# Kernel optimization log

Measured on AMD Instinct MI355X. Metric: run time of the kernel, lower is better.

The kernel has to match this reference:

```python
import jax, jax.numpy as jnp
import numpy as np

B, N, IN_DIM, HID, HEADS, K = 2, 2048, 1024, 512, 8, 8
HD = HID // HEADS
EPS = 1e-5
SCALE = float(1.0 / np.sqrt(HD))

def _ln(x, g, b):
    m = jnp.mean(x, -1, keepdims=True)
    v = jnp.var(x, -1, keepdims=True)
    return (x - m) * jax.lax.rsqrt(v + EPS) * g + b

def setup_inputs() -> dict:
    key = jax.random.key(0)
    ks = jax.random.split(key, 40)
    def p(k, shape):
        return jax.random.normal(k, shape, jnp.float32) * 0.02
    z = lambda *s: jnp.zeros(s, jnp.float32)
    o = lambda *s: jnp.ones(s, jnp.float32)
    return {
        "x": jax.random.normal(ks[0], (B, N, IN_DIM), jnp.float32),
        # fc_start: Linear(in,hid) + GLU Linear(hid,2*hid)
        "w_start": p(ks[1], (HID, IN_DIM)), "b_start": z(HID),
        "glu_w": p(ks[2], (2 * HID, HID)), "glu_b": z(2 * HID),
        # 2 GCN layers (stacked on leading axis)
        "gcn_w": p(ks[3], (2, HID, HID)), "gcn_b": z(2, HID),
        "gcn_g": o(2, HID), "gcn_beta": z(2, HID),
        # 2 transformer layers
        "qkv_w": p(ks[4], (2, 3 * HID, HID)), "qkv_b": z(2, 3 * HID),
        "out_w": p(ks[5], (2, HID, HID)), "out_b": z(2, HID),
        "ln1_g": o(2, HID), "ln1_b": z(2, HID),
        "ffn_w1": p(ks[6], (2, 2 * HID, HID)), "ffn_b1": z(2, 2 * HID),
        "ffn_w2": p(ks[7], (2, HID, 2 * HID)), "ffn_b2": z(2, HID),
        "ln2_g": o(2, HID), "ln2_b": z(2, HID),
        # fusion, attention pooling, classifier
        "fus_w": p(ks[8], (HID, 2 * HID)), "fus_b": z(HID),
        "attn_w1": p(ks[9], (256, HID)), "attn_b1": z(256),
        "attn_w2": p(ks[10], (1, 256)), "attn_b2": z(1),
        "cls_w1": p(ks[11], (HID // 2, HID)), "cls_b1": z(HID // 2),
        "cls_w2": p(ks[12], (1, HID // 2)), "cls_b2": z(1),
    }

def reference(x, w_start, b_start, glu_w, glu_b, gcn_w, gcn_b, gcn_g, gcn_beta,
              qkv_w, qkv_b, out_w, out_b, ln1_g, ln1_b, ffn_w1, ffn_b1,
              ffn_w2, ffn_b2, ln2_g, ln2_b, fus_w, fus_b,
              attn_w1, attn_b1, attn_w2, attn_b2,
              cls_w1, cls_b1, cls_w2, cls_b2):
    # fc_start: Linear -> GLU (dropout off in eval)
    h = x @ w_start.T + b_start
    vg = h @ glu_w.T + glu_b
    val, gate = jnp.split(vg, 2, -1)
    h = val * jax.nn.sigmoid(gate)                      # [B,N,HID]

    # dynamic KNN graph: cdist + topk + scatter + sym-normalize
    sq = jnp.sum(h * h, -1)
    d2 = sq[:, :, None] + sq[:, None, :] - 2.0 * jnp.einsum('bnc,bmc->bnm', h, h)
    dist = jnp.sqrt(jnp.maximum(d2, 0.0))
    _, idx = jax.lax.top_k(-dist, K + 1)                # nearest K+1 (incl self)
    bi = jnp.arange(B)[:, None, None]
    ri = jnp.arange(N)[None, :, None]
    adj = jnp.zeros((B, N, N), h.dtype).at[bi, ri, idx].set(1.0)
    rs = jnp.sum(adj, -1)
    dinv = jnp.where(rs > 0, rs ** -0.5, 0.0)
    adj = adj * dinv[:, :, None] * dinv[:, None, :]     # == D^-1/2 A D^-1/2

    # GCN branch
    hg = h
    for i in range(2):
        s = hg @ gcn_w[i].T + gcn_b[i]
        o = jnp.einsum('bnm,bmc->bnc', adj, s)
        o = _ln(o, gcn_g[i], gcn_beta[i])
        hg = jax.nn.leaky_relu(o, 0.2) + hg

    # Transformer branch (post-LN)
    ht = h
    for i in range(2):
        qkv = ht @ qkv_w[i].T + qkv_b[i]
        q, k_, v = jnp.split(qkv, 3, -1)
        q = q.reshape(B, N, HEADS, HD)
        k_ = k_.reshape(B, N, HEADS, HD)
        v = v.reshape(B, N, HEADS, HD)
        att = jax.nn.softmax(jnp.einsum('bqhd,bkhd->bhqk', q, k_) * SCALE, -1)
        ao = jnp.einsum('bhqk,bkhd->bqhd', att, v).reshape(B, N, HID)
        ao = ao @ out_w[i].T + out_b[i]
        ht = _ln(ht + ao, ln1_g[i], ln1_b[i])
        ff = jax.nn.gelu(ht @ ffn_w1[i].T + ffn_b1[i], approximate=False) @ ffn_w2[i].T + ffn_b2[i]
        ht = _ln(ht + ff, ln2_g[i], ln2_b[i])

    hf = jnp.concatenate([hg, ht], -1) @ fus_w.T + fus_b  # [B,N,HID]

    # gated attention pooling
    a = jnp.tanh(hf @ attn_w1.T + attn_b1) @ attn_w2.T + attn_b2
    a = jax.nn.softmax(a, axis=1)                       # [B,N,1]
    M = jnp.sum(hf * a, axis=1)                         # [B,HID]

    logits = jax.nn.elu(M @ cls_w1.T + cls_b1) @ cls_w2.T + cls_b2  # [B,1]
    return logits, a, M
```

## Files before the change

### kernel.cpp

```cpp
#include <hip/hip_runtime.h>
#include <hip/hip_bf16.h>
#include <math.h>

#define NSEQ 2048
#define ROWS 4096
#define KNN 9
#define MB (1ull << 20)

typedef short bh8 __attribute__((ext_vector_type(8)));
typedef float f4v __attribute__((ext_vector_type(4)));
typedef unsigned long long u64k;

__device__ __forceinline__ short f2bf(float f) {
    union { float f; unsigned u; } v; v.f = f;
    unsigned r = (v.u + 0x7fffu + ((v.u >> 16) & 1u)) >> 16;
    return (short)r;
}
__device__ __forceinline__ float b2f(short s) {
    union { unsigned u; float f; } v; v.u = ((unsigned)(unsigned short)s) << 16; return v.f;
}

__device__ __forceinline__ void gload16(const void* g, void* l) {
    __builtin_amdgcn_global_load_lds(
        (const __attribute__((address_space(1))) void*)g,
        (__attribute__((address_space(3))) void*)l, 16, 0, 0);
}

__device__ __forceinline__ float blockReduceSum(float v, float* red) {
    int tid = threadIdx.x;
    red[tid] = v; __syncthreads();
    for (int s = 128; s > 0; s >>= 1) {
        if (tid < s) red[tid] += red[tid + s];
        __syncthreads();
    }
    float r = red[0]; __syncthreads();
    return r;
}

struct CvtArgs { const float* src[10]; short* dst[10]; int n4[10]; };
__global__ __launch_bounds__(256) void cvt_k(CvtArgs a) {
    int s = blockIdx.y;
    const float* sp = a.src[s]; short* dp = a.dst[s]; int n = a.n4[s];
    for (int i = blockIdx.x * 256 + threadIdx.x; i < n; i += gridDim.x * 256) {
        float4 v = ((const float4*)sp)[i];
        short4 o; o.x = f2bf(v.x); o.y = f2bf(v.y); o.z = f2bf(v.z); o.w = f2bf(v.w);
        ((short4*)dp)[i] = o;
    }
}

template <int OUTMODE>
__global__ __launch_bounds__(256) void mfma_gemm(
        const short* __restrict__ A, const short* __restrict__ W,
        const float* __restrict__ bias, float* __restrict__ Cf, short* __restrict__ Cb,
        int M, int N, int K)
{
    __shared__ short As[2][64 * 64];
    __shared__ short Bs[2][64 * 64];
    int tid = threadIdx.x;
    int wv = tid >> 6, l = tid & 63;
    int g = l >> 4, c = l & 15;
    int wr = wv >> 1, wc = wv & 1;
    int bm = blockIdx.y * 64, bn = blockIdx.x * 64;
    int sr = l >> 3, sc = ((l & 7) ^ sr) * 8;
    const short* Ap = A + (size_t)(bm + wv * 16 + sr) * K + sc;
    const short* Wp = W + (size_t)(bn + wv * 16 + sr) * K + sc;
    int ldsB = (wv * 16) * 64;

    #define GSTAGE(buf, k0) { \
        gload16(Ap + (k0), &As[buf][ldsB]); \
        gload16(Ap + (size_t)8 * K + (k0), &As[buf][ldsB + 8 * 64]); \
        gload16(Wp + (k0), &Bs[buf][ldsB]); \
        gload16(Wp + (size_t)8 * K + (k0), &Bs[buf][ldsB + 8 * 64]); }

    f4v acc[2][2] = {};
    GSTAGE(0, 0);
    __syncthreads();
    int nk = K >> 6;
    for (int t = 0; t < nk; ++t) {
        int cur = t & 1;
        if (t + 1 < nk) GSTAGE(cur ^ 1, (t + 1) << 6);
        #pragma unroll
        for (int ks = 0; ks < 2; ++ks) {
            bh8 af[2], bf_[2];
            #pragma unroll
            for (int mi = 0; mi < 2; ++mi) {
                int row = wr * 32 + mi * 16 + c;
                af[mi] = *(const bh8*)(&As[cur][row * 64 + (((ks * 4 + g) ^ (c & 7)) * 8)]);
            }
            #pragma unroll
            for (int ni = 0; ni < 2; ++ni) {
                int row = wc * 32 + ni * 16 + c;
                bf_[ni] = *(const bh8*)(&Bs[cur][row * 64 + (((ks * 4 + g) ^ (c & 7)) * 8)]);
            }
            #pragma unroll
            for (int mi = 0; mi < 2; ++mi)
                #pragma unroll
                for (int ni = 0; ni < 2; ++ni)
                    acc[mi][ni] = __builtin_amdgcn_mfma_f32_16x16x32_bf16(af[mi], bf_[ni], acc[mi][ni], 0, 0, 0);
        }
        __syncthreads();
    }
    #undef GSTAGE
    short* Kb_  = (OUTMODE == 3) ? Cb + 2097152 : nullptr;
    short* Vt_  = (OUTMODE == 3) ? Cb + 4194304 : nullptr;
    #pragma unroll
    for (int mi = 0; mi < 2; ++mi) {
        int row = bm + wr * 32 + mi * 16 + g * 4;
        #pragma unroll
        for (int ni = 0; ni < 2; ++ni) {
            int col = bn + wc * 32 + ni * 16 + c;
            float bv = bias[col];
            if (OUTMODE == 3) {
                int b = row >> 11, n0 = row & 2047;
                if (col < 512) {
                    int h = col >> 6, d = col & 63;
                    size_t base = (((size_t)(b * 8 + h) * NSEQ + n0) << 6) + d;
                    #pragma unroll
                    for (int rr = 0; rr < 4; ++rr)
                        Cb[base + ((size_t)rr << 6)] = f2bf((acc[mi][ni][rr] + bv) * 0.18033688f);
                } else if (col < 1024) {
                    int cc = col - 512, h = cc >> 6, d = cc & 63;
                    size_t base = (((size_t)(b * 8 + h) * NSEQ + n0) << 6) + d;
                    #pragma unroll
                    for (int rr = 0; rr < 4; ++rr)
                        Kb_[base + ((size_t)rr << 6)] = f2bf(acc[mi][ni][rr] + bv);
                } else {
                    int cc = col - 1024, h = cc >> 6, d = cc & 63;
                    short4 ov;
                    ov.x = f2bf(acc[mi][ni][0] + bv);
                    ov.y = f2bf(acc[mi][ni][1] + bv);
                    ov.z = f2bf(acc[mi][ni][2] + bv);
                    ov.w = f2bf(acc[mi][ni][3] + bv);
                    *(short4*)(Vt_ + (((size_t)((b * 8 + h) * 64 + d)) << 11) + n0) = ov;
                }
            } else {
                #pragma unroll
                for (int rr = 0; rr < 4; ++rr) {
                    float v = acc[mi][ni][rr] + bv;
                    if (OUTMODE == 0) Cf[(size_t)(row + rr) * N + col] = v;
                    else if (OUTMODE == 1) Cb[(size_t)(row + rr) * N + col] = f2bf(v);
                    else if (OUTMODE == 2) {
                        Cf[(size_t)(row + rr) * N + col] = v;
                        Cb[(size_t)(row + rr) * N + col] = f2bf(v);
                    } else if (OUTMODE == 4) {
                        Cb[(size_t)(row + rr) * N + col] = f2bf(0.5f * v * (1.f + erff(v * 0.70710678118654752f)));
                    } else if (OUTMODE == 5) {
                        Cf[(size_t)(row + rr) * N + col] = tanhf(v);
                    }
                }
            }
        }
    }
}

__global__ __launch_bounds__(256) void mfma_gram(
        const short* __restrict__ Hi, const short* __restrict__ Lo,
        const float* __restrict__ SQ, float* __restrict__ D2)
{
    __shared__ short HiR[64 * 64], LoR[64 * 64], HiC[64 * 64], LoC[64 * 64];
    int tid = threadIdx.x;
    int wv = tid >> 6, l = tid & 63;
    int g = l >> 4, c = l & 15;
    int wr = wv >> 1, wc = wv & 1;
    int bm = blockIdx.y * 64, bn = blockIdx.x * 64;
    int sr = l >> 3, sc = ((l & 7) ^ sr) * 8;
    const short* hiR = Hi + (size_t)(bm + wv * 16 + sr) * 512 + sc;
    const short* loR = Lo + (size_t)(bm + wv * 16 + sr) * 512 + sc;
    const short* hiC = Hi + (size_t)(bn + wv * 16 + sr) * 512 + sc;
    const short* loC = Lo + (size_t)(bn + wv * 16 + sr) * 512 + sc;
    int ldsOff = (wv * 16) * 64;
    f4v acc[2][2] = {};
    for (int k0 = 0; k0 < 512; k0 += 64) {
        __syncthreads();
        gload16(hiR + k0, HiR + ldsOff);
        gload16(hiR + (size_t)8 * 512 + k0, HiR + ldsOff + 8 * 64);
        gload16(loR + k0, LoR + ldsOff);
        gload16(loR + (size_t)8 * 512 + k0, LoR + ldsOff + 8 * 64);
        gload16(hiC + k0, HiC + ldsOff);
        gload16(hiC + (size_t)8 * 512 + k0, HiC + ldsOff + 8 * 64);
        gload16(loC + k0, LoC + ldsOff);
        gload16(loC + (size_t)8 * 512 + k0, LoC + ldsOff + 8 * 64);
        __syncthreads();
        #pragma unroll
        for (int ks = 0; ks < 2; ++ks) {
            bh8 hr[2], lr_[2], hc[2], lc[2];
            #pragma unroll
            for (int mi = 0; mi < 2; ++mi) {
                int o = (wr * 32 + mi * 16 + c) * 64 + (((ks * 4 + g) ^ (c & 7)) * 8);
                hr[mi] = *(const bh8*)(HiR + o);
                lr_[mi] = *(const bh8*)(LoR + o);
            }
            #pragma unroll
            for (int ni = 0; ni < 2; ++ni) {
                int o = (wc * 32 + ni * 16 + c) * 64 + (((ks * 4 + g) ^ (c & 7)) * 8);
                hc[ni] = *(const bh8*)(HiC + o);
                lc[ni] = *(const bh8*)(LoC + o);
            }
            #pragma unroll
            for (int mi = 0; mi < 2; ++mi)
                #pragma unroll
                for (int ni = 0; ni < 2; ++ni) {
                    acc[mi][ni] = __builtin_amdgcn_mfma_f32_16x16x32_bf16(hr[mi], hc[ni], acc[mi][ni], 0, 0, 0);
                    acc[mi][ni] = __builtin_amdgcn_mfma_f32_16x16x32_bf16(hr[mi], lc[ni], acc[mi][ni], 0, 0, 0);
                    acc[mi][ni] = __builtin_amdgcn_mfma_f32_16x16x32_bf16(lr_[mi], hc[ni], acc[mi][ni], 0, 0, 0);
                }
        }
    }
    #pragma unroll
    for (int mi = 0; mi < 2; ++mi) {
        int row = bm + wr * 32 + mi * 16 + g * 4;
        #pragma unroll
        for (int ni = 0; ni < 2; ++ni) {
            int col = bn + wc * 32 + ni * 16 + c;
            float sqc = SQ[col];
            #pragma unroll
            for (int rr = 0; rr < 4; ++rr)
                D2[(size_t)(row + rr) * NSEQ + col] = SQ[row + rr] + sqc - 2.f * acc[mi][ni][rr];
        }
    }
}

__global__ __launch_bounds__(256) void topk9_k(const float* __restrict__ D2, int* __restrict__ idx)
{
    int n = blockIdx.x, tid = threadIdx.x;
    __shared__ u64k lists[256][9];
    u64k a[8];
    union { float f; unsigned u; } cv;
    #pragma unroll
    for (int j = 0; j < 8; ++j) {
        int mcol = tid + j * 256;
        cv.f = fmaxf(D2[(size_t)n * NSEQ + mcol], 0.f);
        a[j] = ((u64k)cv.u << 32) | (unsigned)mcol;
    }
    #define CE(i,j) { u64k x = a[i], y = a[j]; bool t = x < y; a[i] = t ? x : y; a[j] = t ? y : x; }
    CE(0,1) CE(2,3) CE(4,5) CE(6,7)
    CE(0,2) CE(1,3) CE(4,6) CE(5,7)
    CE(1,2) CE(5,6)
    CE(0,4) CE(1,5) CE(2,6) CE(3,7)
    CE(2,4) CE(3,5)
    CE(1,2) CE(3,4) CE(5,6)
    #undef CE
    #pragma unroll
    for (int j = 0; j < 8; ++j) lists[tid][j] = a[j];
    lists[tid][8] = ~0ull;
    __syncthreads();
    for (int s = 128; s >= 1; s >>= 1) {
        if (tid < s) {
            u64k out[9];
            u64k* Al = lists[tid];
            u64k* Bl = lists[tid + s];
            int ia = 0, ib = 0;
            #pragma unroll
            for (int o = 0; o < 9; ++o) {
                u64k av = Al[ia], bv = Bl[ib];
                bool t = av <= bv;
                out[o] = t ? av : bv;
                ia += t; ib += !t;
            }
            #pragma unroll
            for (int o = 0; o < 9; ++o) Al[o] = out[o];
        }
        __syncthreads();
    }
    if (tid < 9) idx[n * KNN + tid] = (int)(lists[0][tid] & 0xffffffffu);
}

__global__ __launch_bounds__(256) void gcn_post(
        const float* __restrict__ s, const int* __restrict__ idx,
        const float* __restrict__ g, const float* __restrict__ be,
        float* __restrict__ hg, short* __restrict__ hgb)
{
    int row = blockIdx.x, tid = threadIdx.x;
    int bb = row >> 11;
    __shared__ float os[512];
    __shared__ float red[256];
    int id[KNN];
    #pragma unroll
    for (int j = 0; j < KNN; ++j) id[j] = idx[row * KNN + j] + (bb << 11);
    for (int c = tid; c < 512; c += 256) {
        float acc = 0.f;
        #pragma unroll
        for (int j = 0; j < KNN; ++j) acc += s[((size_t)id[j] << 9) + c];
        os[c] = acc * (1.f / 9.f);
    }
    __syncthreads();
    float mean = blockReduceSum(os[tid] + os[tid + 256], red) * (1.f / 512.f);
    float d0 = os[tid] - mean, d1 = os[tid + 256] - mean;
    float var = blockReduceSum(d0 * d0 + d1 * d1, red) * (1.f / 512.f);
    float rs = rsqrtf(var + 1e-5f);
    size_t base = (size_t)row << 9;
    for (int c = tid; c < 512; c += 256) {
        float y = (os[c] - mean) * rs * g[c] + be[c];
        y = y > 0.f ? y : 0.2f * y;
        float nv = y + hg[base + c];
        hg[base + c] = nv;
        hgb[base + c] = f2bf(nv);
    }
}

__global__ __launch_bounds__(256) void ln_res(
        float* __restrict__ x, const float* __restrict__ r,
        const float* __restrict__ g, const float* __restrict__ b, short* __restrict__ xb)
{
    int row = blockIdx.x, tid = threadIdx.x;
    __shared__ float xs[512];
    __shared__ float red[256];
    size_t base = (size_t)row << 9;
    for (int c = tid; c < 512; c += 256) xs[c] = x[base + c] + r[base + c];
    __syncthreads();
    float mean = blockReduceSum(xs[tid] + xs[tid + 256], red) * (1.f / 512.f);
    float d0 = xs[tid] - mean, d1 = xs[tid + 256] - mean;
    float var = blockReduceSum(d0 * d0 + d1 * d1, red) * (1.f / 512.f);
    float rs = rsqrtf(var + 1e-5f);
    for (int c = tid; c < 512; c += 256) {
        float y = (xs[c] - mean) * rs * g[c] + b[c];
        x[base + c] = y;
        xb[base + c] = f2bf(y);
    }
}

__global__ __launch_bounds__(256) void flash_attn(
        const short* __restrict__ Qb, const short* __restrict__ Kb,
        const short* __restrict__ Vt, float* __restrict__ Op, float* __restrict__ Ml)
{
    __shared__ short Ks[2][4096];
    __shared__ short Vs[2][4096];
    int tid = threadIdx.x;
    int wid = tid >> 6, lane = tid & 63;
    int g = lane >> 4, c = lane & 15;
    int s = blockIdx.y, bh = blockIdx.z;
    int q0 = blockIdx.x * 64 + wid * 16;
    int srow = lane >> 3;
    int sc8 = ((lane & 7) ^ srow) * 8;
    int w8 = wid * 8;

    const short* KbB = Kb + ((size_t)bh * NSEQ + s * (NSEQ / 2)) * 64;
    const short* VtB = Vt + (size_t)bh * 64 * NSEQ + s * (NSEQ / 2);

    const short* qbase = Qb + ((size_t)bh * NSEQ + q0 + c) * 64 + g * 8;
    bh8 qa0 = *(const bh8*)(qbase);
    bh8 qa1 = *(const bh8*)(qbase + 32);

    f4v o0 = {0,0,0,0}, o1 = {0,0,0,0}, o2 = {0,0,0,0}, o3 = {0,0,0,0};
    float lloc = 0.f;
    float mrun = -INFINITY;
    int hi2 = g >> 1;
    int s1 = c + (((g << 1) & 3) << 4);
    int s2 = c + ((((g << 1) + 1) & 3) << 4);

    #define FSTAGE(buf, kt) { \
        const short* kp_ = KbB + (size_t)(kt) * 64 * 64; \
        gload16(kp_ + (size_t)(w8 + srow) * 64 + sc8,        &Ks[buf][w8 * 64]); \
        gload16(kp_ + (size_t)(32 + w8 + srow) * 64 + sc8,   &Ks[buf][(32 + w8) * 64]); \
        const short* vp_ = VtB + (size_t)(kt) * 64; \
        gload16(vp_ + (size_t)(w8 + srow) * NSEQ + sc8,      &Vs[buf][w8 * 64]); \
        gload16(vp_ + (size_t)(32 + w8 + srow) * NSEQ + sc8, &Vs[buf][(32 + w8) * 64]); }

    FSTAGE(0, 0);
    __syncthreads();
    for (int t = 0; t < 16; ++t) {
        int cur = t & 1;
        if (t < 15) FSTAGE(cur ^ 1, t + 1);
        f4v sv[4];
        #pragma unroll
        for (int cb = 0; cb < 4; ++cb) {
            int row = cb * 16 + c;
            const short* kr = &Ks[cur][row * 64];
            bh8 kb0 = *(const bh8*)(kr + ((g ^ (row & 7)) * 8));
            bh8 kb1 = *(const bh8*)(kr + (((4 + g) ^ (row & 7)) * 8));
            f4v a = {0,0,0,0};
            a = __builtin_amdgcn_mfma_f32_16x16x32_bf16(kb0, qa0, a, 0, 0, 0);
            a = __builtin_amdgcn_mfma_f32_16x16x32_bf16(kb1, qa1, a, 0, 0, 0);
            sv[cb] = a;
        }
        float mt = fmaxf(fmaxf(fmaxf(sv[0][0], sv[0][1]), fmaxf(sv[0][2], sv[0][3])),
                         fmaxf(fmaxf(sv[1][0], sv[1][1]), fmaxf(sv[1][2], sv[1][3])));
        mt = fmaxf(mt, fmaxf(fmaxf(sv[2][0], sv[2][1]), fmaxf(sv[2][2], sv[2][3])));
        mt = fmaxf(mt, fmaxf(fmaxf(sv[3][0], sv[3][1]), fmaxf(sv[3][2], sv[3][3])));
        mt = fmaxf(mt, __shfl_xor(mt, 16));
        mt = fmaxf(mt, __shfl_xor(mt, 32));
        if (__any(mt > mrun + 6.f)) {
            float mn = fmaxf(mrun, mt);
            float al = __builtin_amdgcn_exp2f(mrun - mn);
            mrun = mn;
            o0 *= al; o1 *= al; o2 *= al; o3 *= al; lloc *= al;
        }
        unsigned wv_[8];
        #pragma unroll
        for (int cb = 0; cb < 4; ++cb) {
            float p0 = __builtin_amdgcn_exp2f(sv[cb][0] - mrun);
            float p1 = __builtin_amdgcn_exp2f(sv[cb][1] - mrun);
            float p2 = __builtin_amdgcn_exp2f(sv[cb][2] - mrun);
            float p3 = __builtin_amdgcn_exp2f(sv[cb][3] - mrun);
            lloc += (p0 + p1) + (p2 + p3);
            asm("v_cvt_pk_bf16_f32 %0, %1, %2" : "=v"(wv_[cb * 2])     : "v"(p0), "v"(p1));
            asm("v_cvt_pk_bf16_f32 %0, %1, %2" : "=v"(wv_[cb * 2 + 1]) : "v"(p2), "v"(p3));
        }
        union { unsigned u[4]; bh8 h; } pa0u, pa1u;
        {
            unsigned t0 = __shfl((int)wv_[0], s1), t2 = __shfl((int)wv_[2], s1);
            unsigned t1 = __shfl((int)wv_[1], s1), t3 = __shfl((int)wv_[3], s1);
            unsigned u0 = __shfl((int)wv_[0], s2), u2 = __shfl((int)wv_[2], s2);
            unsigned u1 = __shfl((int)wv_[1], s2), u3 = __shfl((int)wv_[3], s2);
            pa0u.u[0] = hi2 ? t2 : t0;
            pa0u.u[1] = hi2 ? t3 : t1;
            pa0u.u[2] = hi2 ? u2 : u0;
            pa0u.u[3] = hi2 ? u3 : u1;
        }
        {
            unsigned t0 = __shfl((int)wv_[4], s1), t2 = __shfl((int)wv_[6], s1);
            unsigned t1 = __shfl((int)wv_[5], s1), t3 = __shfl((int)wv_[7], s1);
            unsigned u0 = __shfl((int)wv_[4], s2), u2 = __shfl((int)wv_[6], s2);
            unsigned u1 = __shfl((int)wv_[5], s2), u3 = __shfl((int)wv_[7], s2);
            pa1u.u[0] = hi2 ? t2 : t0;
            pa1u.u[1] = hi2 ? t3 : t1;
            pa1u.u[2] = hi2 ? u2 : u0;
            pa1u.u[3] = hi2 ? u3 : u1;
        }
        #pragma unroll
        for (int db = 0; db < 4; ++db) {
            int row = db * 16 + c;
            const short* vr = &Vs[cur][row * 64];
            bh8 vb0 = *(const bh8*)(vr + ((g ^ (row & 7)) * 8));
            bh8 vb1 = *(const bh8*)(vr + (((4 + g) ^ (row & 7)) * 8));
            f4v* op = (db == 0) ? &o0 : (db == 1) ? &o1 : (db == 2) ? &o2 : &o3;
            *op = __builtin_amdgcn_mfma_f32_16x16x32_bf16(vb0, pa0u.h, *op, 0, 0, 0);
            *op = __builtin_amdgcn_mfma_f32_16x16x32_bf16(vb1, pa1u.h, *op, 0, 0, 0);
        }
        __syncthreads();
    }
    #undef FSTAGE
    float lsum = lloc;
    lsum += __shfl_xor(lsum, 16);
    lsum += __shfl_xor(lsum, 32);
    size_t qrow = ((size_t)(s * 16 + bh) * NSEQ) + q0 + c;
    size_t rb = qrow * 64 + g * 4;
    #pragma unroll
    for (int r = 0; r < 4; ++r) {
        Op[rb + r]      = o0[r];
        Op[rb + 16 + r] = o1[r];
        Op[rb + 32 + r] = o2[r];
        Op[rb + 48 + r] = o3[r];
    }
    if (g == 0) {
        Ml[qrow * 2]     = mrun;
        Ml[qrow * 2 + 1] = lsum;
    }
}

__global__ __launch_bounds__(256) void merge_k(const float* __restrict__ Op, const float* __restrict__ Ml,
                                               short* __restrict__ aob)
{
    int idx = blockIdx.x * 256 + threadIdx.x;
    int d = idx & 63, q = (idx >> 6) & 2047, bh = idx >> 17;
    size_t r0 = (size_t)bh * NSEQ + q;
    size_t r1 = (size_t)(16 + bh) * NSEQ + q;
    float m0 = Ml[r0 * 2], l0 = Ml[r0 * 2 + 1];
    float m1 = Ml[r1 * 2], l1 = Ml[r1 * 2 + 1];
    float M = fmaxf(m0, m1);
    float w0 = __builtin_amdgcn_exp2f(m0 - M), w1 = __builtin_amdgcn_exp2f(m1 - M);
    float L = l0 * w0 + l1 * w1;
    float v = (Op[r0 * 64 + d] * w0 + Op[r1 * 64 + d] * w1) / L;
    int b = bh >> 3, h = bh & 7;
    aob[((size_t)(b * NSEQ + q)) * 512 + h * 64 + d] = f2bf(v);
}

__global__ __launch_bounds__(256) void glu_row_k(const float* __restrict__ vg, float* __restrict__ h,
        float* __restrict__ hgf, short* __restrict__ hi, short* __restrict__ lo,
        float* __restrict__ sq) {
    int row = blockIdx.x, tid = threadIdx.x;
    __shared__ float red[256];
    size_t vb = (size_t)row << 10;
    size_t hb = (size_t)row << 9;
    float ss = 0.f;
    #pragma unroll
    for (int j = 0; j < 2; ++j) {
        int c = tid + j * 256;
        float v = vg[vb + c], gt = vg[vb + 512 + c];
        float hv = v * (1.f / (1.f + __expf(-gt)));
        h[hb + c] = hv; hgf[hb + c] = hv;
        short hbb = f2bf(hv);
        hi[hb + c] = hbb;
        lo[hb + c] = f2bf(hv - b2f(hbb));
        ss = fmaf(hv, hv, ss);
    }
    float sm = blockReduceSum(ss, red);
    if (tid == 0) sq[row] = sm;
}

__global__ void concat_bf(const short* __restrict__ hgb, const short* __restrict__ htb,
                          short* __restrict__ cat) {
    for (int i = blockIdx.x * 256 + threadIdx.x; i < ROWS * 256; i += gridDim.x * 256) {
        int row = i >> 8, c4 = (i & 255) * 4;
        short4 v = (c4 < 512) ? *(const short4*)(hgb + ((size_t)row << 9) + c4)
                              : *(const short4*)(htb + ((size_t)row << 9) + c4 - 512);
        *(short4*)(cat + ((size_t)row << 10) + c4) = v;
    }
}

__global__ __launch_bounds__(256) void rowdot_k(const float* __restrict__ t, const float* __restrict__ w2,
                                                const float* __restrict__ b2, float* __restrict__ srow) {
    int row = blockIdx.x, tid = threadIdx.x;
    __shared__ float red[256];
    float s = blockReduceSum(t[(size_t)row * 256 + tid] * w2[tid], red);
    if (tid == 0) srow[row] = s + b2[0];
}
__global__ __launch_bounds__(256) void softmax_n_k(const float* __restrict__ srow, float* __restrict__ a,
                                                   float* __restrict__ out) {
    int b = blockIdx.x, tid = threadIdx.x;
    __shared__ float red[256];
    float mx = -INFINITY;
    for (int n = tid; n < NSEQ; n += 256) mx = fmaxf(mx, srow[b * NSEQ + n]);
    red[tid] = mx; __syncthreads();
    for (int s = 128; s > 0; s >>= 1) {
        if (tid < s) red[tid] = fmaxf(red[tid], red[tid + s]);
        __syncthreads();
    }
    mx = red[0]; __syncthreads();
    float sm = 0.f;
    for (int n = tid; n < NSEQ; n += 256) {
        float e = expf(srow[b * NSEQ + n] - mx);
        a[b * NSEQ + n] = e; sm += e;
    }
    float inv = 1.f / blockReduceSum(sm, red);
    for (int n = tid; n < NSEQ; n += 256) {
        float v = a[b * NSEQ + n] * inv;
        a[b * NSEQ + n] = v;
        out[2 + b * NSEQ + n] = v;
    }
}
__global__ __launch_bounds__(256) void pool_part(const float* __restrict__ hf, const float* __restrict__ a,
                                                 float* __restrict__ part) {
    int b = blockIdx.y, chunk = blockIdx.x, tid = threadIdx.x;
    float a0 = 0.f, a1 = 0.f;
    for (int r = 0; r < 64; ++r) {
        int n = chunk * 64 + r;
        float wgt = a[b * NSEQ + n];
        const float* row = hf + ((size_t)(b * NSEQ + n) << 9);
        a0 = fmaf(row[tid], wgt, a0);
        a1 = fmaf(row[tid + 256], wgt, a1);
    }
    part[((b * 32 + chunk) << 9) + tid] = a0;
    part[((b * 32 + chunk) << 9) + tid + 256] = a1;
}
__global__ __launch_bounds__(256) void pool_fin(const float* __restrict__ part, float* __restrict__ Mb,
                                                float* __restrict__ out) {
    int b = blockIdx.x, tid = threadIdx.x;
    float s0 = 0.f, s1 = 0.f;
    for (int ch = 0; ch < 32; ++ch) {
        s0 += part[((b * 32 + ch) << 9) + tid];
        s1 += part[((b * 32 + ch) << 9) + tid + 256];
    }
    Mb[b * 512 + tid] = s0; Mb[b * 512 + tid + 256] = s1;
    out[2 + ROWS + b * 512 + tid] = s0; out[2 + ROWS + b * 512 + tid + 256] = s1;
}
__global__ __launch_bounds__(256) void classifier_k(const float* __restrict__ Mb,
        const float* __restrict__ w1, const float* __restrict__ b1,
        const float* __restrict__ w2, const float* __restrict__ b2, float* __restrict__ out) {
    int b = blockIdx.x, tid = threadIdx.x;
    __shared__ float Ms[512];
    __shared__ float red[256];
    for (int c = tid; c < 512; c += 256) Ms[c] = Mb[b * 512 + c];
    __syncthreads();
    float acc = 0.f;
    for (int c = 0; c < 512; ++c) acc = fmaf(Ms[c], w1[tid * 512 + c], acc);
    acc += b1[tid];
    float hj = acc > 0.f ? acc : expm1f(acc);
    float s = blockReduceSum(hj * w2[tid], red);
    if (tid == 0) out[b] = s + b2[0];
}

extern "C" void kernel_launch(void* const* d_in, const int* in_sizes, int n_in,
                              void* d_out, int out_size, void* d_ws, size_t ws_size,
                              hipStream_t stream)
{
    const float* X      = (const float*)d_in[0];
    const float* Wstart = (const float*)d_in[1];
    const float* Bstart = (const float*)d_in[2];
    const float* GluW   = (const float*)d_in[3];
    const float* GluB   = (const float*)d_in[4];
    const float* GcnW   = (const float*)d_in[5];
    const float* GcnB   = (const float*)d_in[6];
    const float* GcnG   = (const float*)d_in[7];
    const float* GcnBe  = (const float*)d_in[8];
    const float* QkvW   = (const float*)d_in[9];
    const float* QkvB   = (const float*)d_in[10];
    const float* OutW   = (const float*)d_in[11];
    const float* OutB   = (const float*)d_in[12];
    const float* Ln1G   = (const float*)d_in[13];
    const float* Ln1B   = (const float*)d_in[14];
    const float* Ffn1W  = (const float*)d_in[15];
    const float* Ffn1B  = (const float*)d_in[16];
    const float* Ffn2W  = (const float*)d_in[17];
    const float* Ffn2B  = (const float*)d_in[18];
    const float* Ln2G   = (const float*)d_in[19];
    const float* Ln2B   = (const float*)d_in[20];
    const float* FusW   = (const float*)d_in[21];
    const float* FusB   = (const float*)d_in[22];
    const float* AW1    = (const float*)d_in[23];
    const float* AB1    = (const float*)d_in[24];
    const float* AW2    = (const float*)d_in[25];
    const float* AB2    = (const float*)d_in[26];
    const float* CW1    = (const float*)d_in[27];
    const float* CB1    = (const float*)d_in[28];
    const float* CW2    = (const float*)d_in[29];
    const float* CB2    = (const float*)d_in[30];
    float* out = (float*)d_out;

    if (ws_size < 86 * MB) return;

    char* w = (char*)d_ws;
    short* Wb = (short*)w;
    short* wbStart = Wb;
    short* wbGlu   = Wb + 524288;
    short* wbGcn   = Wb + 1048576;
    short* wbQkv   = Wb + 1572864;
    short* wbOut   = Wb + 3145728;
    short* wbFfn1  = Wb + 3670016;
    short* wbFfn2  = Wb + 4718592;
    short* wbFus   = Wb + 5767168;
    short* wbAw1   = Wb + 6291456;
    float* sq   = (float*)(w + 13 * MB);
    int*   idx  = (int*)  (w + 13 * MB + (16u << 10));
    float* srow = (float*)(w + 13 * MB + (176u << 10));
    float* afb  = (float*)(w + 13 * MB + (192u << 10));
    float* Mbuf = (float*)(w + 13 * MB + (208u << 10));
    float* part = (float*)(w + 13 * MB + (212u << 10));
    float* Ml   = (float*)(w + 13 * MB + (384u << 10));
    short* Xbf  = (short*)(w + 14 * MB);
    float* hg   = (float*)(w + 14 * MB);
    short* hpreb= (short*)(w + 22 * MB);
    short* hgb  = (short*)(w + 22 * MB);
    float* big  = (float*)(w + 26 * MB);
    float* ffn2o= (float*)(w + 42 * MB);
    float* h    = (float*)(w + 50 * MB);
    short* hhi  = (short*)(w + 58 * MB);
    short* hlo  = (short*)(w + 62 * MB);
    short* htb  = (short*)(w + 62 * MB);
    float* hf   = (float*)(w + 58 * MB);
    short* hfb  = (short*)(w + 66 * MB);
    short* aob  = (short*)(w + 70 * MB);
    float* t256 = (float*)(w + 70 * MB);
    short* Qb   = (short*)(w + 74 * MB);
    short* Kb   = (short*)(w + 78 * MB);
    short* Vt   = (short*)(w + 82 * MB);
    short* ffb  = (short*)(w + 74 * MB);
    short* catb = (short*)(w + 74 * MB);

    dim3 blk(256);

    CvtArgs ca;
    ca.src[0] = X;     ca.dst[0] = Xbf;     ca.n4[0] = ROWS * 1024 / 4;
    ca.src[1] = Wstart;ca.dst[1] = wbStart; ca.n4[1] = 524288 / 4;
    ca.src[2] = GluW;  ca.dst[2] = wbGlu;   ca.n4[2] = 524288 / 4;
    ca.src[3] = GcnW;  ca.dst[3] = wbGcn;   ca.n4[3] = 524288 / 4;
    ca.src[4] = QkvW;  ca.dst[4] = wbQkv;   ca.n4[4] = 1572864 / 4;
    ca.src[5] = OutW;  ca.dst[5] = wbOut;   ca.n4[5] = 524288 / 4;
    ca.src[6] = Ffn1W; ca.dst[6] = wbFfn1;  ca.n4[6] = 1048576 / 4;
    ca.src[7] = Ffn2W; ca.dst[7] = wbFfn2;  ca.n4[7] = 1048576 / 4;
    ca.src[8] = FusW;  ca.dst[8] = wbFus;   ca.n4[8] = 524288 / 4;
    ca.src[9] = AW1;   ca.dst[9] = wbAw1;   ca.n4[9] = 131072 / 4;
    cvt_k<<<dim3(256, 10), blk, 0, stream>>>(ca);

    mfma_gemm<1><<<dim3(8, 64), blk, 0, stream>>>(Xbf, wbStart, Bstart, nullptr, hpreb, ROWS, 512, 1024);
    mfma_gemm<0><<<dim3(16, 64), blk, 0, stream>>>(hpreb, wbGlu, GluB, big, nullptr, ROWS, 1024, 512);
    glu_row_k<<<dim3(ROWS), blk, 0, stream>>>(big, h, hg, hhi, hlo, sq);

    for (int b = 0; b < 2; ++b) {
        mfma_gram<<<dim3(32, 32), blk, 0, stream>>>(hhi + (size_t)b * NSEQ * 512,
                                                    hlo + (size_t)b * NSEQ * 512,
                                                    sq + b * NSEQ, big);
        topk9_k<<<dim3(NSEQ), blk, 0, stream>>>(big, idx + b * NSEQ * KNN);
    }

    const short* gA = hhi;
    for (int i = 0; i < 2; ++i) {
        mfma_gemm<0><<<dim3(8, 64), blk, 0, stream>>>(gA, wbGcn + (size_t)i * 262144,
                                                      GcnB + i * 512, big, nullptr, ROWS, 512, 512);
        gcn_post<<<dim3(ROWS), blk, 0, stream>>>(big, idx, GcnG + i * 512, GcnBe + i * 512, hg, hgb);
        gA = hgb;
    }

    const short* tA = hhi;
    for (int i = 0; i < 2; ++i) {
        mfma_gemm<3><<<dim3(24, 64), blk, 0, stream>>>(tA, wbQkv + (size_t)i * 786432,
                                                       QkvB + i * 1536, nullptr, Qb, ROWS, 1536, 512);
        flash_attn<<<dim3(32, 2, 16), blk, 0, stream>>>(Qb, Kb, Vt, big, Ml);
        merge_k<<<dim3(8192), blk, 0, stream>>>(big, Ml, aob);
        mfma_gemm<0><<<dim3(8, 64), blk, 0, stream>>>(aob, wbOut + (size_t)i * 262144,
                                                      OutB + i * 512, big, nullptr, ROWS, 512, 512);
        ln_res<<<dim3(ROWS), blk, 0, stream>>>(h, big, Ln1G + i * 512, Ln1B + i * 512, htb);
        mfma_gemm<4><<<dim3(16, 64), blk, 0, stream>>>(htb, wbFfn1 + (size_t)i * 524288,
                                                       Ffn1B + i * 1024, nullptr, ffb, ROWS, 1024, 512);
        mfma_gemm<0><<<dim3(8, 64), blk, 0, stream>>>(ffb, wbFfn2 + (size_t)i * 524288,
                                                      Ffn2B + i * 512, ffn2o, nullptr, ROWS, 512, 1024);
        ln_res<<<dim3(ROWS), blk, 0, stream>>>(h, ffn2o, Ln2G + i * 512, Ln2B + i * 512, htb);
        tA = htb;
    }

    concat_bf<<<dim3(2048), blk, 0, stream>>>(hgb, htb, catb);
    mfma_gemm<2><<<dim3(8, 64), blk, 0, stream>>>(catb, wbFus, FusB, hf, hfb, ROWS, 512, 1024);

    mfma_gemm<5><<<dim3(4, 64), blk, 0, stream>>>(hfb, wbAw1, AB1, t256, nullptr, ROWS, 256, 512);
    rowdot_k<<<dim3(ROWS), blk, 0, stream>>>(t256, AW2, AB2, srow);
    softmax_n_k<<<dim3(2), blk, 0, stream>>>(srow, afb, out);
    pool_part<<<dim3(32, 2), blk, 0, stream>>>(hf, afb, part);
    pool_fin<<<dim3(2), blk, 0, stream>>>(part, Mbuf, out);

    classifier_k<<<dim3(2), blk, 0, stream>>>(Mbuf, CW1, CB1, CW2, CB2, out);
}
```

Before: 437.1 us.

## Add 128x128 GEMM tile, split attention KV four ways with bf16 partials

Result: slower. 505.2 us (+15.6%).

```diff
diff --git a/kernel.cpp b/kernel.cpp
--- a/kernel.cpp
+++ b/kernel.cpp
@@ -45,6 +45,49 @@
         float4 v = ((const float4*)sp)[i];
         short4 o; o.x = f2bf(v.x); o.y = f2bf(v.y); o.z = f2bf(v.z); o.w = f2bf(v.w);
         ((short4*)dp)[i] = o;
+    }
+}
+
+template <int OUTMODE>
+__device__ __forceinline__ void gemm_epilogue(int row, int col, int N, const f4v& a,
+        float bv, float* Cf, short* Cb, short* Kb_, short* Vt_)
+{
+    if (OUTMODE == 3) {
+        int b = row >> 11, n0 = row & 2047;
+        if (col < 512) {
+            int h = col >> 6, d = col & 63;
+            size_t base = (((size_t)(b * 8 + h) * NSEQ + n0) << 6) + d;
+            #pragma unroll
+            for (int rr = 0; rr < 4; ++rr)
+                Cb[base + ((size_t)rr << 6)] = f2bf((a[rr] + bv) * 0.18033688f);
+        } else if (col < 1024) {
+            int cc = col - 512, h = cc >> 6, d = cc & 63;
+            size_t base = (((size_t)(b * 8 + h) * NSEQ + n0) << 6) + d;
+            #pragma unroll
+            for (int rr = 0; rr < 4; ++rr)
+                Kb_[base + ((size_t)rr << 6)] = f2bf(a[rr] + bv);
+        } else {
+            int cc = col - 1024, h = cc >> 6, d = cc & 63;
+            short4 ov;
+            ov.x = f2bf(a[0] + bv); ov.y = f2bf(a[1] + bv);
+            ov.z = f2bf(a[2] + bv); ov.w = f2bf(a[3] + bv);
+            *(short4*)(Vt_ + (((size_t)((b * 8 + h) * 64 + d)) << 11) + n0) = ov;
+        }
+    } else {
+        #pragma unroll
+        for (int rr = 0; rr < 4; ++rr) {
+            float v = a[rr] + bv;
+            if (OUTMODE == 0) Cf[(size_t)(row + rr) * N + col] = v;
+            else if (OUTMODE == 1) Cb[(size_t)(row + rr) * N + col] = f2bf(v);
+            else if (OUTMODE == 2) {
+                Cf[(size_t)(row + rr) * N + col] = v;
+                Cb[(size_t)(row + rr) * N + col] = f2bf(v);
+            } else if (OUTMODE == 4) {
+                Cb[(size_t)(row + rr) * N + col] = f2bf(0.5f * v * (1.f + erff(v * 0.70710678118654752f)));
+            } else if (OUTMODE == 5) {
+                Cf[(size_t)(row + rr) * N + col] = tanhf(v);
+            }
+        }
     }
 }
 
@@ -101,54 +144,85 @@
         __syncthreads();
     }
     #undef GSTAGE
-    short* Kb_  = (OUTMODE == 3) ? Cb + 2097152 : nullptr;
-    short* Vt_  = (OUTMODE == 3) ? Cb + 4194304 : nullptr;
+    short* Kb_ = (OUTMODE == 3) ? Cb + 2097152 : nullptr;
+    short* Vt_ = (OUTMODE == 3) ? Cb + 4194304 : nullptr;
     #pragma unroll
     for (int mi = 0; mi < 2; ++mi) {
         int row = bm + wr * 32 + mi * 16 + g * 4;
         #pragma unroll
         for (int ni = 0; ni < 2; ++ni) {
             int col = bn + wc * 32 + ni * 16 + c;
-            float bv = bias[col];
-            if (OUTMODE == 3) {
-                int b = row >> 11, n0 = row & 2047;
-                if (col < 512) {
-                    int h = col >> 6, d = col & 63;
-                    size_t base = (((size_t)(b * 8 + h) * NSEQ + n0) << 6) + d;
-                    #pragma unroll
-                    for (int rr = 0; rr < 4; ++rr)
-                        Cb[base + ((size_t)rr << 6)] = f2bf((acc[mi][ni][rr] + bv) * 0.18033688f);
-                } else if (col < 1024) {
-                    int cc = col - 512, h = cc >> 6, d = cc & 63;
-                    size_t base = (((size_t)(b * 8 + h) * NSEQ + n0) << 6) + d;
-                    #pragma unroll
-                    for (int rr = 0; rr < 4; ++rr)
-                        Kb_[base + ((size_t)rr << 6)] = f2bf(acc[mi][ni][rr] + bv);
-                } else {
-                    int cc = col - 1024, h = cc >> 6, d = cc & 63;
-                    short4 ov;
-                    ov.x = f2bf(acc[mi][ni][0] + bv);
-                    ov.y = f2bf(acc[mi][ni][1] + bv);
-                    ov.z = f2bf(acc[mi][ni][2] + bv);
-                    ov.w = f2bf(acc[mi][ni][3] + bv);
-                    *(short4*)(Vt_ + (((size_t)((b * 8 + h) * 64 + d)) << 11) + n0) = ov;
-                }
-            } else {
+            gemm_epilogue<OUTMODE>(row, col, N, acc[mi][ni], bias[col], Cf, Cb, Kb_, Vt_);
+        }
+    }
+}
+
+template <int OUTMODE>
+__global__ __launch_bounds__(256) void mfma_gemm_big(
+        const short* __restrict__ A, const short* __restrict__ W,
+        const float* __restrict__ bias, float* __restrict__ Cf, short* __restrict__ Cb,
+        int M, int N, int K)
+{
+    __shared__ short As[2][128 * 64];
+    __shared__ short Bs[2][128 * 64];
+    int tid = threadIdx.x;
+    int wv = tid >> 6, l = tid & 63;
+    int g = l >> 4, c = l & 15;
+    int wr = wv >> 1, wc = wv & 1;
+    int bm = blockIdx.y * 128, bn = blockIdx.x * 128;
+    int sr = l >> 3, sc = ((l & 7) ^ sr) * 8;
+    const short* Ap = A + (size_t)(bm + wv * 32 + sr) * K + sc;
+    const short* Wp = W + (size_t)(bn + wv * 32 + sr) * K + sc;
+    int ldsB = (wv * 32) * 64;
+
+    #define GSTAGE(buf, k0) { \
+        gload16(Ap + (k0),                   &As[buf][ldsB]); \
+        gload16(Ap + (size_t) 8 * K + (k0),  &As[buf][ldsB + 8 * 64]); \
+        gload16(Ap + (size_t)16 * K + (k0),  &As[buf][ldsB + 16 * 64]); \
+        gload16(Ap + (size_t)24 * K + (k0),  &As[buf][ldsB + 24 * 64]); \
+        gload16(Wp + (k0),                   &Bs[buf][ldsB]); \
+        gload16(Wp + (size_t) 8 * K + (k0),  &Bs[buf][ldsB + 8 * 64]); \
+        gload16(Wp + (size_t)16 * K + (k0),  &Bs[buf][ldsB + 16 * 64]); \
+        gload16(Wp + (size_t)24 * K + (k0),  &Bs[buf][ldsB + 24 * 64]); }
+
+    f4v acc[4][4] = {};
+    GSTAGE(0, 0);
+    __syncthreads();
+    int nk = K >> 6;
+    for (int t = 0; t < nk; ++t) {
+        int cur = t & 1;
+        if (t + 1 < nk) GSTAGE(cur ^ 1, (t + 1) << 6);
+        #pragma unroll
+        for (int ks = 0; ks < 2; ++ks) {
+            bh8 af[4], bf_[4];
+            #pragma unroll
+            for (int mi = 0; mi < 4; ++mi) {
+                int row = wr * 64 + mi * 16 + c;
+                af[mi] = *(const bh8*)(&As[cur][row * 64 + (((ks * 4 + g) ^ (c & 7)) * 8)]);
+            }
+            #pragma unroll
+            for (int ni = 0; ni < 4; ++ni) {
+                int row = wc * 64 + ni * 16 + c;
+                bf_[ni] = *(const bh8*)(&Bs[cur][row * 64 + (((ks * 4 + g) ^ (c & 7)) * 8)]);
+            }
+            #pragma unroll
+            for (int mi = 0; mi < 4; ++mi)
                 #pragma unroll
-                for (int rr = 0; rr < 4; ++rr) {
-                    float v = acc[mi][ni][rr] + bv;
-                    if (OUTMODE == 0) Cf[(size_t)(row + rr) * N + col] = v;
-                    else if (OUTMODE == 1) Cb[(size_t)(row + rr) * N + col] = f2bf(v);
-                    else if (OUTMODE == 2) {
-                        Cf[(size_t)(row + rr) * N + col] = v;
-                        Cb[(size_t)(row + rr) * N + col] = f2bf(v);
-                    } else if (OUTMODE == 4) {
-                        Cb[(size_t)(row + rr) * N + col] = f2bf(0.5f * v * (1.f + erff(v * 0.70710678118654752f)));
-                    } else if (OUTMODE == 5) {
-                        Cf[(size_t)(row + rr) * N + col] = tanhf(v);
-                    }
-                }
-            }
+                for (int ni = 0; ni < 4; ++ni)
+                    acc[mi][ni] = __builtin_amdgcn_mfma_f32_16x16x32_bf16(af[mi], bf_[ni], acc[mi][ni], 0, 0, 0);
+        }
+        __syncthreads();
+    }
+    #undef GSTAGE
+    short* Kb_ = (OUTMODE == 3) ? Cb + 2097152 : nullptr;
+    short* Vt_ = (OUTMODE == 3) ? Cb + 4194304 : nullptr;
+    #pragma unroll
+    for (int mi = 0; mi < 4; ++mi) {
+        int row = bm + wr * 64 + mi * 16 + g * 4;
+        #pragma unroll
+        for (int ni = 0; ni < 4; ++ni) {
+            int col = bn + wc * 64 + ni * 16 + c;
+            gemm_epilogue<OUTMODE>(row, col, N, acc[mi][ni], bias[col], Cf, Cb, Kb_, Vt_);
         }
     }
 }
@@ -321,7 +395,7 @@
 
 __global__ __launch_bounds__(256) void flash_attn(
         const short* __restrict__ Qb, const short* __restrict__ Kb,
-        const short* __restrict__ Vt, float* __restrict__ Op, float* __restrict__ Ml)
+        const short* __restrict__ Vt, short* __restrict__ Opb, float* __restrict__ Ml)
 {
     __shared__ short Ks[2][4096];
     __shared__ short Vs[2][4096];
@@ -334,8 +408,8 @@
     int sc8 = ((lane & 7) ^ srow) * 8;
     int w8 = wid * 8;
 
-    const short* KbB = Kb + ((size_t)bh * NSEQ + s * (NSEQ / 2)) * 64;
-    const short* VtB = Vt + (size_t)bh * 64 * NSEQ + s * (NSEQ / 2);
+    const short* KbB = Kb + ((size_t)bh * NSEQ + s * 512) * 64;
+    const short* VtB = Vt + (size_t)bh * 64 * NSEQ + s * 512;
 
     const short* qbase = Qb + ((size_t)bh * NSEQ + q0 + c) * 64 + g * 8;
     bh8 qa0 = *(const bh8*)(qbase);
@@ -358,9 +432,9 @@
 
     FSTAGE(0, 0);
     __syncthreads();
-    for (int t = 0; t < 16; ++t) {
+    for (int t = 0; t < 8; ++t) {
         int cur = t & 1;
-        if (t < 15) FSTAGE(cur ^ 1, t + 1);
+        if (t < 7) FSTAGE(cur ^ 1, t + 1);
         f4v sv[4];
         #pragma unroll
         for (int cb = 0; cb < 4; ++cb) {
@@ -437,10 +511,10 @@
     size_t rb = qrow * 64 + g * 4;
     #pragma unroll
     for (int r = 0; r < 4; ++r) {
-        Op[rb + r]      = o0[r];
-        Op[rb + 16 + r] = o1[r];
-        Op[rb + 32 + r] = o2[r];
-        Op[rb + 48 + r] = o3[r];
+        Opb[rb + r]      = f2bf(o0[r]);
+        Opb[rb + 16 + r] = f2bf(o1[r]);
+        Opb[rb + 32 + r] = f2bf(o2[r]);
+        Opb[rb + 48 + r] = f2bf(o3[r]);
     }
     if (g == 0) {
         Ml[qrow * 2]     = mrun;
@@ -448,21 +522,28 @@
     }
 }
 
-__global__ __launch_bounds__(256) void merge_k(const float* __restrict__ Op, const float* __restrict__ Ml,
+__global__ __launch_bounds__(256) void merge_k(const short* __restrict__ Opb, const float* __restrict__ Ml,
                                                short* __restrict__ aob)
 {
     int idx = blockIdx.x * 256 + threadIdx.x;
     int d = idx & 63, q = (idx >> 6) & 2047, bh = idx >> 17;
-    size_t r0 = (size_t)bh * NSEQ + q;
-    size_t r1 = (size_t)(16 + bh) * NSEQ + q;
-    float m0 = Ml[r0 * 2], l0 = Ml[r0 * 2 + 1];
-    float m1 = Ml[r1 * 2], l1 = Ml[r1 * 2 + 1];
-    float M = fmaxf(m0, m1);
-    float w0 = __builtin_amdgcn_exp2f(m0 - M), w1 = __builtin_amdgcn_exp2f(m1 - M);
-    float L = l0 * w0 + l1 * w1;
-    float v = (Op[r0 * 64 + d] * w0 + Op[r1 * 64 + d] * w1) / L;
+    float M = -INFINITY;
+    float mv[4], lv[4];
+    #pragma unroll
+    for (int s = 0; s < 4; ++s) {
+        size_t r = (size_t)(s * 16 + bh) * NSEQ + q;
+        mv[s] = Ml[r * 2]; lv[s] = Ml[r * 2 + 1];
+        M = fmaxf(M, mv[s]);
+    }
+    float L = 0.f, num = 0.f;
+    #pragma unroll
+    for (int s = 0; s < 4; ++s) {
+        float w = __builtin_amdgcn_exp2f(mv[s] - M);
+        L += lv[s] * w;
+        num += b2f(Opb[((size_t)(s * 16 + bh) * NSEQ + q) * 64 + d]) * w;
+    }
     int b = bh >> 3, h = bh & 7;
-    aob[((size_t)(b * NSEQ + q)) * 512 + h * 64 + d] = f2bf(v);
+    aob[((size_t)(b * NSEQ + q)) * 512 + h * 64 + d] = f2bf(num / L);
 }
 
 __global__ __launch_bounds__(256) void glu_row_k(const float* __restrict__ vg, float* __restrict__ h,
@@ -626,12 +707,13 @@
     float* afb  = (float*)(w + 13 * MB + (192u << 10));
     float* Mbuf = (float*)(w + 13 * MB + (208u << 10));
     float* part = (float*)(w + 13 * MB + (212u << 10));
-    float* Ml   = (float*)(w + 13 * MB + (384u << 10));
     short* Xbf  = (short*)(w + 14 * MB);
     float* hg   = (float*)(w + 14 * MB);
     short* hpreb= (short*)(w + 22 * MB);
     short* hgb  = (short*)(w + 22 * MB);
     float* big  = (float*)(w + 26 * MB);
+    short* Opb  = (short*)(w + 26 * MB);
+    float* Ml   = (float*)(w + 42 * MB);
     float* ffn2o= (float*)(w + 42 * MB);
     float* h    = (float*)(w + 50 * MB);
     short* hhi  = (short*)(w + 58 * MB);
@@ -663,7 +745,7 @@
     cvt_k<<<dim3(256, 10), blk, 0, stream>>>(ca);
 
     mfma_gemm<1><<<dim3(8, 64), blk, 0, stream>>>(Xbf, wbStart, Bstart, nullptr, hpreb, ROWS, 512, 1024);
-    mfma_gemm<0><<<dim3(16, 64), blk, 0, stream>>>(hpreb, wbGlu, GluB, big, nullptr, ROWS, 1024, 512);
+    mfma_gemm_big<0><<<dim3(8, 32), blk, 0, stream>>>(hpreb, wbGlu, GluB, big, nullptr, ROWS, 1024, 512);
     glu_row_k<<<dim3(ROWS), blk, 0, stream>>>(big, h, hg, hhi, hlo, sq);
 
     for (int b = 0; b < 2; ++b) {
@@ -683,15 +765,15 @@
 
     const short* tA = hhi;
     for (int i = 0; i < 2; ++i) {
-        mfma_gemm<3><<<dim3(24, 64), blk, 0, stream>>>(tA, wbQkv + (size_t)i * 786432,
-                                                       QkvB + i * 1536, nullptr, Qb, ROWS, 1536, 512);
-        flash_attn<<<dim3(32, 2, 16), blk, 0, stream>>>(Qb, Kb, Vt, big, Ml);
-        merge_k<<<dim3(8192), blk, 0, stream>>>(big, Ml, aob);
+        mfma_gemm_big<3><<<dim3(12, 32), blk, 0, stream>>>(tA, wbQkv + (size_t)i * 786432,
+                                                           QkvB + i * 1536, nullptr, Qb, ROWS, 1536, 512);
+        flash_attn<<<dim3(32, 4, 16), blk, 0, stream>>>(Qb, Kb, Vt, Opb, Ml);
+        merge_k<<<dim3(8192), blk, 0, stream>>>(Opb, Ml, aob);
         mfma_gemm<0><<<dim3(8, 64), blk, 0, stream>>>(aob, wbOut + (size_t)i * 262144,
                                                       OutB + i * 512, big, nullptr, ROWS, 512, 512);
         ln_res<<<dim3(ROWS), blk, 0, stream>>>(h, big, Ln1G + i * 512, Ln1B + i * 512, htb);
-        mfma_gemm<4><<<dim3(16, 64), blk, 0, stream>>>(htb, wbFfn1 + (size_t)i * 524288,
-                                                       Ffn1B + i * 1024, nullptr, ffb, ROWS, 1024, 512);
+        mfma_gemm_big<4><<<dim3(8, 32), blk, 0, stream>>>(htb, wbFfn1 + (size_t)i * 524288,
+                                                          Ffn1B + i * 1024, nullptr, ffb, ROWS, 1024, 512);
         mfma_gemm<0><<<dim3(8, 64), blk, 0, stream>>>(ffb, wbFfn2 + (size_t)i * 524288,
                                                       Ffn2B + i * 512, ffn2o, nullptr, ROWS, 512, 1024);
         ln_res<<<dim3(ROWS), blk, 0, stream>>>(h, ffn2o, Ln2G + i * 512, Ln2B + i * 512, htb);
```
